# Optimization experiments

Hardware: AMD Instinct MI355X
Metric: run time of the kernel (lower is better)

Reference implementation:

```python
import jax, jax.numpy as jnp
import numpy as np

B, L, D, H = 4, 1024, 768, 12
DH = D // H  # 64


def setup_inputs() -> dict:
    key = jax.random.key(0)
    kx, kk, kq, kv = jax.random.split(key, 4)
    # Original uses torch.rand (uniform [0,1)); scale by 1/D so pre-softmax
    # logits stay in a numerically sane range (same math, better conditioning).
    scale = 1.0 / D
    x = jax.random.normal(kx, (B, L, D), dtype=jnp.float32)
    k = jax.random.uniform(kk, (H, D, D), dtype=jnp.float32) * scale
    q = jax.random.uniform(kq, (H, D, D), dtype=jnp.float32) * scale
    v = jax.random.uniform(kv, (H, DH, D), dtype=jnp.float32) * scale
    return {"x": x, "k": k, "q": q, "v": v}


def reference(x, k, q, v):
    # x: [B, L, D]; torch permutes to [B, D, L] then 'bdl,ncd->bncl';
    # equivalent directly: 'bld,ncd->bncl'.
    K = jnp.einsum('bld,ncd->bncl', x, k)   # [B, H, D, L]
    Q = jnp.einsum('bld,ncd->bncl', x, q)   # [B, H, D, L]
    V = jnp.einsum('bld,ncd->bncl', x, v)   # [B, H, DH, L]
    scores = jnp.einsum('bndl,bndm->bnlm', Q, K)        # [B, H, L, L]
    S = jax.nn.softmax(scores, axis=-1)                  # softmax over dim 3
    R = jnp.einsum('bnkl,bndl->bndk', S, V)              # [B, H, DH, L]
    R = R.reshape(x.shape[0], D, -1)                     # [B, D, L]
    return jnp.transpose(R, (0, 2, 1))                   # [B, L, D]
```

## Files before the change

kernel.cpp:

```cpp
#include <hip/hip_runtime.h>
#include <hip/hip_bf16.h>
#include <stdint.h>
#include <stddef.h>

typedef unsigned short u16;
typedef __attribute__((ext_vector_type(8))) short short8;
typedef __attribute__((ext_vector_type(4))) float f32x4;
typedef __attribute__((ext_vector_type(16))) float f32x16;

#define NB 4
#define NL 1024
#define ND 768
#define NH 12
#define NDH 64

__device__ __forceinline__ u16 f2bf(float f) {
  __hip_bfloat16 h = __float2bfloat16(f);
  return *reinterpret_cast<u16*>(&h);
}
__device__ __forceinline__ float bf2f(u16 u) {
  __hip_bfloat16 h;
  *reinterpret_cast<u16*>(&h) = u;
  return __bfloat162float(h);
}

__device__ __forceinline__ void load16_to_lds(const u16* g, u16* l) {
  __builtin_amdgcn_global_load_lds(
      (__attribute__((address_space(1))) void*)(uintptr_t)g,
      (__attribute__((address_space(3))) void*)(uint32_t)(uintptr_t)l,
      16, 0, 0);
}

__global__ __launch_bounds__(256) void cast2_bf16_kernel(const float* __restrict__ inA,
                                                         u16* __restrict__ outA, int n4A,
                                                         const float* __restrict__ inB,
                                                         u16* __restrict__ outB, int n4B) {
  int i = blockIdx.x * 256 + threadIdx.x;
  int stride = gridDim.x * 256;
  int tot = n4A + n4B;
  for (; i < tot; i += stride) {
    const float4* src;
    ushort4* dst;
    int j;
    if (i < n4A) { src = (const float4*)inA; dst = (ushort4*)outA; j = i; }
    else         { src = (const float4*)inB; dst = (ushort4*)outB; j = i - n4A; }
    float4 f = src[j];
    ushort4 o;
    o.x = f2bf(f.x); o.y = f2bf(f.y); o.z = f2bf(f.z); o.w = f2bf(f.w);
    dst[j] = o;
  }
}

__global__ __launch_bounds__(256) void transpose_cast2_kernel(const float* __restrict__ qI,
                                                              const float* __restrict__ kI,
                                                              u16* __restrict__ qT,
                                                              u16* __restrict__ kTp) {
  __shared__ float tile[32][33];
  int hz = blockIdx.z;
  int h = (hz < NH) ? hz : hz - NH;
  const float* src = ((hz < NH) ? qI : kI) + (size_t)h * ND * ND;
  u16* dst = ((hz < NH) ? qT : kTp) + (size_t)h * ND * ND;
  int c0 = blockIdx.x * 32, r0 = blockIdx.y * 32;
  int tx = threadIdx.x & 31, ty = threadIdx.x >> 5;
#pragma unroll
  for (int i = 0; i < 32; i += 8)
    tile[ty + i][tx] = src[(size_t)(r0 + ty + i) * ND + c0 + tx];
  __syncthreads();
  int p = tx & 15, j = (tx >> 4) * 8 + ty;
#pragma unroll
  for (int i = 0; i < 32; i += 16) {
    ushort2 o;
    o.x = f2bf(tile[2 * p][j + i]);
    o.y = f2bf(tile[2 * p + 1][j + i]);
    *(ushort2*)&dst[(size_t)(c0 + j + i) * ND + r0 + 2 * p] = o;
  }
}

template <bool BF16_OUT, int IM, int IN, int KDIM, int LDC>
__global__ __launch_bounds__(256, 4) void gemm_bt(
    const u16* __restrict__ A, const u16* __restrict__ Bm, void* __restrict__ Cv,
    long sAb, long sAn, long sAz,
    long sBb, long sBn, long sBz,
    long sCb, long sCn, long sCz,
    int p0) {
  constexpr int BK = 64;
  constexpr int MTILE = IM * 64;
  constexpr int NTILE = IN * 64;
  constexpr int CPR = BK / 8;
  constexpr int ACH = MTILE * CPR / 256;
  constexpr int BCH = NTILE * CPR / 256;
  __shared__ __align__(16) u16 As[MTILE * BK];
  __shared__ __align__(16) u16 Bs[NTILE * BK];

  int id = blockIdx.x + gridDim.x * (blockIdx.y + gridDim.y * blockIdx.z);
  int total = gridDim.x * gridDim.y * gridDim.z;
  int xx, yy, zz;
  if ((total & 7) == 0) {
    int per = total >> 3;
    int wk = (id & 7) * per + (id >> 3);
    xx = wk % gridDim.x;
    int g2 = wk / gridDim.x;
    yy = g2 % gridDim.y;
    zz = g2 / gridDim.y;
  } else {
    xx = blockIdx.x; yy = blockIdx.y; zz = blockIdx.z;
  }

  int g = p0 + zz;
  int b = g / NH, n = g % NH;
  A  += (size_t)b * sAb + (size_t)n * sAn + (size_t)zz * sAz;
  Bm += (size_t)b * sBb + (size_t)n * sBn + (size_t)zz * sBz;
  size_t cOff = (size_t)b * sCb + (size_t)n * sCn + (size_t)zz * sCz;

  int m0 = yy * MTILE, n0 = xx * NTILE;
  int t = threadIdx.x;
  int lane = t & 63, w = t >> 6;
  int m32 = lane & 31, kg = lane >> 5;
  int wm = w >> 1, wn = w & 1;

  const u16* gAb;
  const u16* gBb;
  {
    int r = t / CPR;
    int cc = (t & (CPR - 1)) ^ (r & 7);
    gAb = A + (size_t)(m0 + r) * KDIM + cc * 8;
    gBb = Bm + (size_t)(n0 + r) * KDIM + cc * 8;
  }

  f32x16 acc[IM][IN];
#pragma unroll
  for (int i = 0; i < IM; i++)
#pragma unroll
    for (int j = 0; j < IN; j++)
#pragma unroll
      for (int r = 0; r < 16; r++) acc[i][j][r] = 0.f;

#pragma unroll 1
  for (int k0 = 0; k0 < KDIM; k0 += BK) {
    __syncthreads();
#pragma unroll
    for (int u = 0; u < ACH; u++)
      load16_to_lds(gAb + (size_t)u * 32 * KDIM, &As[(size_t)(u * 256 + w * 64) * 8]);
    gAb += BK;
#pragma unroll
    for (int u = 0; u < BCH; u++)
      load16_to_lds(gBb + (size_t)u * 32 * KDIM, &Bs[(size_t)(u * 256 + w * 64) * 8]);
    gBb += BK;
    __syncthreads();

#pragma unroll
    for (int kc = 0; kc < 2; kc++) {
      short8 af[IM][2], bfr[IN][2];
#pragma unroll
      for (int i = 0; i < IM; i++) {
        int row = wm * (IM * 32) + i * 32 + m32;
#pragma unroll
        for (int h = 0; h < 2; h++) {
          int ck = (kc * 4 + h * 2 + kg) ^ (row & 7);
          af[i][h] = *(const short8*)&As[row * BK + ck * 8];
        }
      }
#pragma unroll
      for (int j = 0; j < IN; j++) {
        int row = wn * (IN * 32) + j * 32 + m32;
#pragma unroll
        for (int h = 0; h < 2; h++) {
          int ck = (kc * 4 + h * 2 + kg) ^ (row & 7);
          bfr[j][h] = *(const short8*)&Bs[row * BK + ck * 8];
        }
      }
#pragma unroll
      for (int i = 0; i < IM; i++)
#pragma unroll
        for (int j = 0; j < IN; j++) {
          acc[i][j] = __builtin_amdgcn_mfma_f32_32x32x16_bf16(af[i][0], bfr[j][0], acc[i][j], 0, 0, 0);
          acc[i][j] = __builtin_amdgcn_mfma_f32_32x32x16_bf16(af[i][1], bfr[j][1], acc[i][j], 0, 0, 0);
        }
    }
  }

#pragma unroll
  for (int i = 0; i < IM; i++) {
#pragma unroll
    for (int j = 0; j < IN; j++) {
      int colg = n0 + wn * (IN * 32) + j * 32 + m32;
#pragma unroll
      for (int r = 0; r < 16; r++) {
        int rowg = m0 + wm * (IM * 32) + i * 32 + (r & 3) + 8 * (r >> 2) + 4 * kg;
        float vv = acc[i][j][r];
        if (BF16_OUT) {
          ((u16*)Cv)[cOff + (size_t)rowg * LDC + colg] = f2bf(vv);
        } else {
          ((float*)Cv)[cOff + (size_t)rowg * LDC + colg] = vv;
        }
      }
    }
  }
}

__global__ __launch_bounds__(256, 4) void gemm_prep(
    const u16* __restrict__ kT, const u16* __restrict__ qT, u16* __restrict__ MTp,
    const u16* __restrict__ vb, const u16* __restrict__ xb, u16* __restrict__ V2p) {
  constexpr int BK = 64;
  constexpr int KDIM = ND;
  constexpr int CPR = BK / 8;
  constexpr long DD = (long)ND * ND;
  constexpr long LD = (long)NL * ND;
  __shared__ __align__(16) u16 As[128 * BK];
  __shared__ __align__(16) u16 Bs[128 * BK];

  int id = blockIdx.x + gridDim.x * (blockIdx.y + gridDim.y * blockIdx.z);
  int total = gridDim.x * gridDim.y * gridDim.z;
  int per = total >> 3;
  int wk = (id & 7) * per + (id >> 3);
  int xx = wk % gridDim.x;
  int g2 = wk / gridDim.x;
  int yy = g2 % gridDim.y;
  int zz = g2 / gridDim.y;

  const u16* A;
  const u16* Bm;
  u16* C;
  int ldc;
  if (zz < NH) {
    if (xx >= 6) return;
    A = kT + (size_t)zz * DD;
    Bm = qT + (size_t)zz * DD;
    C = MTp + (size_t)zz * DD;
    ldc = ND;
  } else {
    int b = zz - NH;
    A = vb;
    Bm = xb + (size_t)b * LD;
    C = V2p + (size_t)b * NH * NDH * NL;
    ldc = NL;
  }

  int m0 = yy * 128, n0 = xx * 128;
  int t = threadIdx.x;
  int lane = t & 63, w = t >> 6;
  int m32 = lane & 31, kg = lane >> 5;
  int wm = w >> 1, wn = w & 1;

  const u16* gAb;
  const u16* gBb;
  {
    int r = t / CPR;
    int cc = (t & (CPR - 1)) ^ (r & 7);
    gAb = A + (size_t)(m0 + r) * KDIM + cc * 8;
    gBb = Bm + (size_t)(n0 + r) * KDIM + cc * 8;
  }

  f32x16 acc[2][2];
#pragma unroll
  for (int i = 0; i < 2; i++)
#pragma unroll
    for (int j = 0; j < 2; j++)
#pragma unroll
      for (int r = 0; r < 16; r++) acc[i][j][r] = 0.f;

#pragma unroll 1
  for (int k0 = 0; k0 < KDIM; k0 += BK) {
    __syncthreads();
#pragma unroll
    for (int u = 0; u < 4; u++)
      load16_to_lds(gAb + (size_t)u * 32 * KDIM, &As[(size_t)(u * 256 + w * 64) * 8]);
    gAb += BK;
#pragma unroll
    for (int u = 0; u < 4; u++)
      load16_to_lds(gBb + (size_t)u * 32 * KDIM, &Bs[(size_t)(u * 256 + w * 64) * 8]);
    gBb += BK;
    __syncthreads();

#pragma unroll
    for (int kc = 0; kc < 2; kc++) {
      short8 af[2][2], bfr[2][2];
#pragma unroll
      for (int i = 0; i < 2; i++) {
        int row = wm * 64 + i * 32 + m32;
#pragma unroll
        for (int h = 0; h < 2; h++) {
          int ck = (kc * 4 + h * 2 + kg) ^ (row & 7);
          af[i][h] = *(const short8*)&As[row * BK + ck * 8];
        }
      }
#pragma unroll
      for (int j = 0; j < 2; j++) {
        int row = wn * 64 + j * 32 + m32;
#pragma unroll
        for (int h = 0; h < 2; h++) {
          int ck = (kc * 4 + h * 2 + kg) ^ (row & 7);
          bfr[j][h] = *(const short8*)&Bs[row * BK + ck * 8];
        }
      }
#pragma unroll
      for (int i = 0; i < 2; i++)
#pragma unroll
        for (int j = 0; j < 2; j++) {
          acc[i][j] = __builtin_amdgcn_mfma_f32_32x32x16_bf16(af[i][0], bfr[j][0], acc[i][j], 0, 0, 0);
          acc[i][j] = __builtin_amdgcn_mfma_f32_32x32x16_bf16(af[i][1], bfr[j][1], acc[i][j], 0, 0, 0);
        }
    }
  }

#pragma unroll
  for (int i = 0; i < 2; i++) {
#pragma unroll
    for (int j = 0; j < 2; j++) {
      int colg = n0 + wn * 64 + j * 32 + m32;
#pragma unroll
      for (int r = 0; r < 16; r++) {
        int rowg = m0 + wm * 64 + i * 32 + (r & 3) + 8 * (r >> 2) + 4 * kg;
        C[(size_t)rowg * ldc + colg] = f2bf(acc[i][j][r]);
      }
    }
  }
}

template <bool BF16_OUT, int KDIM, int LDC>
__global__ __launch_bounds__(512, 2) void gemm256_8p(
    const u16* __restrict__ A, const u16* __restrict__ Bm, void* __restrict__ Cv,
    long sAb, long sAn, long sAz,
    long sBb, long sBn, long sBz,
    long sCb, long sCn, long sCz,
    int p0) {
  constexpr int BK = 64;
  constexpr int NT = KDIM / BK;
  constexpr int NC = NT / 2;
  static_assert(KDIM % 128 == 0 && NC >= 2, "need even #K-tiles and >=2 cycles");
  __shared__ __align__(16) u16 As[2][256 * BK];
  __shared__ __align__(16) u16 Bs[2][256 * BK];

  int id = blockIdx.x + gridDim.x * (blockIdx.y + gridDim.y * blockIdx.z);
  int total = gridDim.x * gridDim.y * gridDim.z;
  int xx, yy, zz;
  if ((total & 7) == 0) {
    int per = total >> 3;
    int wk = (id & 7) * per + (id >> 3);
    xx = wk % gridDim.x;
    int g2 = wk / gridDim.x;
    yy = g2 % gridDim.y;
    zz = g2 / gridDim.y;
  } else {
    xx = blockIdx.x; yy = blockIdx.y; zz = blockIdx.z;
  }

  int g = p0 + zz;
  int b = g / NH, n = g % NH;
  A  += (size_t)b * sAb + (size_t)n * sAn + (size_t)zz * sAz;
  Bm += (size_t)b * sBb + (size_t)n * sBn + (size_t)zz * sBz;
  size_t cOff = (size_t)b * sCb + (size_t)n * sCn + (size_t)zz * sCz;

  int m0 = yy * 256, n0 = xx * 256;
  int t = threadIdx.x;
  int lane = t & 63, w = t >> 6;
  int wm = w >> 2, wn = w & 3;
  int l15 = lane & 15, q4 = lane >> 4;

  int r0 = t >> 3;
  int cc0 = (t & 7) ^ (r0 & 7);
  const u16* gA = A + (size_t)(m0 + r0) * KDIM + cc0 * 8;
  const u16* gB = Bm + (size_t)(n0 + r0) * KDIM + cc0 * 8;
  int wslab = w * 512;

#define STG_A1(d, h, u, kt) load16_to_lds( \
    gA + (size_t)((h) * 128 + (u) * 64) * KDIM + (size_t)(kt) * BK, \
    &As[d][((h) * 128 + (u) * 64) * BK + wslab])
#define STG_B1(d, h, u, kt) load16_to_lds( \
    gB + (size_t)((h) * 128 + (u) * 64) * KDIM + (size_t)(kt) * BK, \
    &Bs[d][((h) * 128 + (u) * 64) * BK + wslab])
#define STG_A2(d, h, kt) do { STG_A1(d, h, 0, kt); STG_A1(d, h, 1, kt); } while (0)
#define STG_B2(d, h, kt) do { STG_B1(d, h, 0, kt); STG_B1(d, h, 1, kt); } while (0)

#define READ_A(d, qm, dst) do { \
  _Pragma("unroll") for (int fm = 0; fm < 4; fm++) { \
    int row = (qm) * 128 + wm * 64 + fm * 16 + l15; \
    _Pragma("unroll") for (int ks = 0; ks < 2; ks++) { \
      int ck = (ks * 4 + q4) ^ (row & 7); \
      dst[fm][ks] = *(const short8*)&As[d][row * BK + ck * 8]; \
    } \
  } \
} while (0)

#define READ_B(d, qn, dst) do { \
  _Pragma("unroll") for (int fn = 0; fn < 2; fn++) { \
    int row = (qn) * 128 + wn * 32 + fn * 16 + l15; \
    _Pragma("unroll") for (int ks = 0; ks < 2; ks++) { \
      int ck = (ks * 4 + q4) ^ (row & 7); \
      dst[fn][ks] = *(const short8*)&Bs[d][row * BK + ck * 8]; \
    } \
  } \
} while (0)

#define MF_Q(qm, qn, AR, BR) do { \
  __builtin_amdgcn_s_setprio(1); \
  _Pragma("unroll") for (int ks = 0; ks < 2; ks++) \
    _Pragma("unroll") for (int fm = 0; fm < 4; fm++) \
      _Pragma("unroll") for (int fn = 0; fn < 2; fn++) \
        acc[qm][qn][fm][fn] = __builtin_amdgcn_mfma_f32_16x16x32_bf16( \
            AR[fm][ks], BR[fn][ks], acc[qm][qn][fm][fn], 0, 0, 0); \
  __builtin_amdgcn_s_setprio(0); \
} while (0)

#define PH_SYNC() do { \
  __builtin_amdgcn_s_barrier(); \
  asm volatile("s_waitcnt lgkmcnt(0)" ::: "memory"); \
  __builtin_amdgcn_sched_barrier(0); \
} while (0)
#define PH_END() do { \
  __builtin_amdgcn_s_barrier(); \
  __builtin_amdgcn_sched_barrier(0); \
} while (0)

  f32x4 acc[2][2][4][2];
#pragma unroll
  for (int qm = 0; qm < 2; qm++)
#pragma unroll
    for (int qn = 0; qn < 2; qn++)
#pragma unroll
      for (int fm = 0; fm < 4; fm++)
#pragma unroll
        for (int fn = 0; fn < 2; fn++)
          acc[qm][qn][fm][fn] = (f32x4){0.f, 0.f, 0.f, 0.f};

  STG_A2(0, 0, 0); STG_A2(0, 1, 0);
  STG_B2(0, 0, 0); STG_B2(0, 1, 0);
  STG_A2(1, 0, 1); STG_B2(1, 0, 1);
  asm volatile("s_waitcnt vmcnt(4)" ::: "memory");
  __builtin_amdgcn_s_barrier();
  __builtin_amdgcn_sched_barrier(0);

#pragma unroll 1
  for (int cyc = 0; cyc < NC; ++cyc) {
    int t0 = cyc * 2;
    bool full = (cyc + 1 < NC);
    short8 af0[4][2], af1[4][2], bq0[2][2], bq1[2][2];

    READ_A(0, 0, af0); READ_B(0, 0, bq0);
    STG_A2(1, 1, t0 + 1);
    PH_SYNC(); MF_Q(0, 0, af0, bq0); PH_END();
    READ_B(0, 1, bq1);
    STG_B2(1, 1, t0 + 1);
    PH_SYNC(); MF_Q(0, 1, af0, bq1); PH_END();
    READ_A(0, 1, af1);
    if (full) STG_A2(0, 0, t0 + 2);
    PH_SYNC(); MF_Q(1, 0, af1, bq0); PH_END();
    if (full) STG_B2(0, 0, t0 + 2);
    __builtin_amdgcn_s_barrier();
    MF_Q(1, 1, af1, bq1);
    __builtin_amdgcn_sched_barrier(0);
    if (full) asm volatile("s_waitcnt vmcnt(4)" ::: "memory");
    else      asm volatile("s_waitcnt vmcnt(0)" ::: "memory");
    PH_END();

    READ_A(1, 0, af0); READ_B(1, 0, bq0);
    if (full) STG_A2(0, 1, t0 + 2);
    PH_SYNC(); MF_Q(0, 0, af0, bq0); PH_END();
    READ_B(1, 1, bq1);
    if (full) STG_B2(0, 1, t0 + 2);
    PH_SYNC(); MF_Q(0, 1, af0, bq1); PH_END();
    READ_A(1, 1, af1);
    if (full) STG_A2(1, 0, t0 + 3);
    PH_SYNC(); MF_Q(1, 0, af1, bq0); PH_END();
    if (full) {
      STG_B2(1, 0, t0 + 3);
      __builtin_amdgcn_s_barrier();
      MF_Q(1, 1, af1, bq1);
      __builtin_amdgcn_sched_barrier(0);
      asm volatile("s_waitcnt vmcnt(4)" ::: "memory");
      PH_END();
    } else {
      __builtin_amdgcn_s_barrier();
      MF_Q(1, 1, af1, bq1);
    }
  }

#pragma unroll
  for (int qm = 0; qm < 2; qm++)
#pragma unroll
    for (int qn = 0; qn < 2; qn++)
#pragma unroll
      for (int fm = 0; fm < 4; fm++)
#pragma unroll
        for (int fn = 0; fn < 2; fn++) {
          int colg = n0 + qn * 128 + wn * 32 + fn * 16 + l15;
#pragma unroll
          for (int r = 0; r < 4; r++) {
            int rowg = m0 + qm * 128 + wm * 64 + fm * 16 + q4 * 4 + r;
            float vv = acc[qm][qn][fm][fn][r];
            if (BF16_OUT) {
              ((u16*)Cv)[cOff + (size_t)rowg * LDC + colg] = f2bf(vv);
            } else {
              ((float*)Cv)[cOff + (size_t)rowg * LDC + colg] = vv;
            }
          }
        }
#undef STG_A1
#undef STG_B1
#undef STG_A2
#undef STG_B2
#undef READ_A
#undef READ_B
#undef MF_Q
#undef PH_SYNC
#undef PH_END
}

__global__ __launch_bounds__(256) void softmax_pv_kernel(
    const u16* __restrict__ Sb, const u16* __restrict__ V2, float* __restrict__ out,
    int p0) {
  __shared__ __align__(16) u16 Ps[64 * 128];
  __shared__ __align__(16) u16 Vs[64 * 128];

  int id = blockIdx.x + gridDim.x * blockIdx.y;
  int total = gridDim.x * gridDim.y;
  int xx, zz;
  if ((total & 7) == 0) {
    int per = total >> 3;
    int wk = (id & 7) * per + (id >> 3);
    xx = wk & 15; zz = wk >> 4;
  } else {
    xx = blockIdx.x; zz = blockIdx.y;
  }

  int g = p0 + zz;
  int b = g / NH, n = g % NH;
  const u16* S = Sb + (size_t)zz * NL * NL;
  const u16* V = V2 + (size_t)g * NDH * NL;

  int l0 = xx * 64;
  int t = threadIdx.x;
  int lane = t & 63, w = t >> 6;
  int row16 = lane & 15, q = lane >> 4;
  int rs = row16 & 7;

  f32x4 acc[5];
#pragma unroll
  for (int j = 0; j < 5; j++) acc[j] = (f32x4){0.f, 0.f, 0.f, 0.f};

  short8 onesf;
  {
    short val = (row16 == 0) ? (short)0x3F80 : (short)0;
#pragma unroll
    for (int e = 0; e < 8; e++) onesf[e] = val;
  }

  const u16* ssrc[4];
  const u16* vsrc[4];
#pragma unroll
  for (int u = 0; u < 4; u++) {
    int c = u * 256 + t;
    int r = c >> 4, cc = (c & 15) ^ (r & 7);
    ssrc[u] = S + (size_t)(l0 + r) * NL + cc * 8;
    vsrc[u] = V + (size_t)r * NL + cc * 8;
  }

#pragma unroll 1
  for (int mt = 0; mt < 8; mt++) {
    int mo = mt * 128;
    __syncthreads();
#pragma unroll
    for (int u = 0; u < 4; u++)
      load16_to_lds(ssrc[u] + mo, &Ps[(size_t)(u * 256 + w * 64) * 8]);
#pragma unroll
    for (int u = 0; u < 4; u++)
      load16_to_lds(vsrc[u] + mo, &Vs[(size_t)(u * 256 + w * 64) * 8]);
    __syncthreads();

#pragma unroll
    for (int kk = 0; kk < 4; kk++) {
      int ch = ((kk * 4 + q) ^ rs) * 16;
      int lrow = w * 16 + row16;
      short8 raw = *(const short8*)((const char*)Ps + lrow * 256 + ch);
      short8 af;
#pragma unroll
      for (int e = 0; e < 8; e++) af[e] = (short)f2bf(__expf(bf2f((u16)raw[e])));
      short8 bfr[4];
#pragma unroll
      for (int j = 0; j < 4; j++) {
        int dh = j * 16 + row16;
        bfr[j] = *(const short8*)((const char*)Vs + dh * 256 + ch);
      }
#pragma unroll
      for (int j = 0; j < 4; j++)
        acc[j] = __builtin_amdgcn_mfma_f32_16x16x32_bf16(af, bfr[j], acc[j], 0, 0, 0);
      acc[4] = __builtin_amdgcn_mfma_f32_16x16x32_bf16(af, onesf, acc[4], 0, 0, 0);
    }
  }

#pragma unroll
  for (int r = 0; r < 4; r++) {
    float sum = __shfl(acc[4][r], lane & 48, 64);
    float inv = 1.0f / sum;
    int row = l0 + w * 16 + q * 4 + r;
    float* op = out + ((size_t)b * NL + row) * ND + n * NDH;
#pragma unroll
    for (int j = 0; j < 4; j++)
      op[j * 16 + row16] = acc[j][r] * inv;
  }
}

extern "C" void kernel_launch(void* const* d_in, const int* in_sizes, int n_in,
                              void* d_out, int out_size, void* d_ws, size_t ws_size,
                              hipStream_t stream) {
  (void)in_sizes; (void)n_in; (void)out_size;
  const float* x  = (const float*)d_in[0];
  const float* kI = (const float*)d_in[1];
  const float* qI = (const float*)d_in[2];
  const float* vI = (const float*)d_in[3];
  float* out = (float*)d_out;

  size_t off = 0;
  char* wsb = (char*)d_ws;
  auto alloc = [&](size_t bytes) -> char* {
    char* p = wsb + off;
    off += (bytes + 255) & ~(size_t)255;
    return p;
  };
  u16* xb = (u16*)alloc((size_t)NB * NL * ND * 2);
  u16* vb = (u16*)alloc((size_t)NH * NDH * ND * 2);
  u16* MT = (u16*)alloc((size_t)NH * ND * ND * 2);
  u16* V2 = (u16*)alloc((size_t)NB * NH * NDH * NL * 2);
  size_t fixedSz = off;

  u16* qT = (u16*)alloc((size_t)NH * ND * ND * 2);
  u16* kT = (u16*)alloc((size_t)NH * ND * ND * 2);
  size_t scratchEndQK = off;

  const size_t Tsz  = (size_t)NL * ND * 2;
  const size_t Ssz  = (size_t)NL * NL * 2;
  const size_t perPair = Tsz + Ssz;

  int chunk = NB * NH;
  {
    size_t avail = ws_size > fixedSz ? ws_size - fixedSz : 0;
    size_t maxChunk = avail / perPair;
    if (maxChunk < 1) maxChunk = 1;
    if (maxChunk < (size_t)chunk) {
      int passes = (int)(((size_t)NB * NH + maxChunk - 1) / maxChunk);
      chunk = (NB * NH + passes - 1) / passes;
    }
  }
  off = fixedSz;
  u16* T  = (u16*)alloc((size_t)chunk * Tsz);
  u16* Sb = (u16*)alloc((size_t)chunk * Ssz);
  if (off < scratchEndQK) off = scratchEndQK;

  const long DD  = (long)ND * ND;
  const long LD  = (long)NL * ND;
  const long LL  = (long)NL * NL;

  {
    int n4A = NB * NL * ND / 4;
    int n4B = NH * NDH * ND / 4;
    cast2_bf16_kernel<<<dim3((n4A + n4B + 255) / 256), dim3(256), 0, stream>>>(
        x, xb, n4A, vI, vb, n4B);
  }
  transpose_cast2_kernel<<<dim3(24, 24, 2 * NH), dim3(256), 0, stream>>>(qI, kI, qT, kT);

  gemm_prep<<<dim3(8, 6, 16), dim3(256), 0, stream>>>(kT, qT, MT, vb, xb, V2);

  for (int p0 = 0; p0 < NB * NH; p0 += chunk) {
    int c = NB * NH - p0;
    if (c > chunk) c = chunk;
    gemm_bt<true, 2, 2, 768, ND><<<dim3(6, 8, c), dim3(256), 0, stream>>>(
        xb, MT, T,
        LD, 0, 0,  0, DD, 0,  0, 0, LD, p0);
    gemm256_8p<true, 768, NL><<<dim3(4, 4, c), dim3(512), 0, stream>>>(
        T, xb, Sb,
        0, 0, LD,  LD, 0, 0,  0, 0, LL, p0);
    softmax_pv_kernel<<<dim3(16, c), dim3(256), 0, stream>>>(Sb, V2, out, p0);
  }
}
```

Baseline: 300.7 us.

## Fuse QK score GEMM into softmax-PV kernel, dropping the score matrix buffer

```diff
diff --git a/kernel.cpp b/kernel.cpp
--- a/kernel.cpp
+++ b/kernel.cpp
@@ -317,198 +317,12 @@
   }
 }
 
-template <bool BF16_OUT, int KDIM, int LDC>
-__global__ __launch_bounds__(512, 2) void gemm256_8p(
-    const u16* __restrict__ A, const u16* __restrict__ Bm, void* __restrict__ Cv,
-    long sAb, long sAn, long sAz,
-    long sBb, long sBn, long sBz,
-    long sCb, long sCn, long sCz,
-    int p0) {
+__global__ __launch_bounds__(256, 2) void qk_softmax_pv(
+    const u16* __restrict__ Tq, const u16* __restrict__ xb, const u16* __restrict__ V2,
+    float* __restrict__ out, int p0) {
   constexpr int BK = 64;
-  constexpr int NT = KDIM / BK;
-  constexpr int NC = NT / 2;
-  static_assert(KDIM % 128 == 0 && NC >= 2, "need even #K-tiles and >=2 cycles");
-  __shared__ __align__(16) u16 As[2][256 * BK];
-  __shared__ __align__(16) u16 Bs[2][256 * BK];
-
-  int id = blockIdx.x + gridDim.x * (blockIdx.y + gridDim.y * blockIdx.z);
-  int total = gridDim.x * gridDim.y * gridDim.z;
-  int xx, yy, zz;
-  if ((total & 7) == 0) {
-    int per = total >> 3;
-    int wk = (id & 7) * per + (id >> 3);
-    xx = wk % gridDim.x;
-    int g2 = wk / gridDim.x;
-    yy = g2 % gridDim.y;
-    zz = g2 / gridDim.y;
-  } else {
-    xx = blockIdx.x; yy = blockIdx.y; zz = blockIdx.z;
-  }
-
-  int g = p0 + zz;
-  int b = g / NH, n = g % NH;
-  A  += (size_t)b * sAb + (size_t)n * sAn + (size_t)zz * sAz;
-  Bm += (size_t)b * sBb + (size_t)n * sBn + (size_t)zz * sBz;
-  size_t cOff = (size_t)b * sCb + (size_t)n * sCn + (size_t)zz * sCz;
-
-  int m0 = yy * 256, n0 = xx * 256;
-  int t = threadIdx.x;
-  int lane = t & 63, w = t >> 6;
-  int wm = w >> 2, wn = w & 3;
-  int l15 = lane & 15, q4 = lane >> 4;
-
-  int r0 = t >> 3;
-  int cc0 = (t & 7) ^ (r0 & 7);
-  const u16* gA = A + (size_t)(m0 + r0) * KDIM + cc0 * 8;
-  const u16* gB = Bm + (size_t)(n0 + r0) * KDIM + cc0 * 8;
-  int wslab = w * 512;
-
-#define STG_A1(d, h, u, kt) load16_to_lds( \
-    gA + (size_t)((h) * 128 + (u) * 64) * KDIM + (size_t)(kt) * BK, \
-    &As[d][((h) * 128 + (u) * 64) * BK + wslab])
-#define STG_B1(d, h, u, kt) load16_to_lds( \
-    gB + (size_t)((h) * 128 + (u) * 64) * KDIM + (size_t)(kt) * BK, \
-    &Bs[d][((h) * 128 + (u) * 64) * BK + wslab])
-#define STG_A2(d, h, kt) do { STG_A1(d, h, 0, kt); STG_A1(d, h, 1, kt); } while (0)
-#define STG_B2(d, h, kt) do { STG_B1(d, h, 0, kt); STG_B1(d, h, 1, kt); } while (0)
-
-#define READ_A(d, qm, dst) do { \
-  _Pragma("unroll") for (int fm = 0; fm < 4; fm++) { \
-    int row = (qm) * 128 + wm * 64 + fm * 16 + l15; \
-    _Pragma("unroll") for (int ks = 0; ks < 2; ks++) { \
-      int ck = (ks * 4 + q4) ^ (row & 7); \
-      dst[fm][ks] = *(const short8*)&As[d][row * BK + ck * 8]; \
-    } \
-  } \
-} while (0)
-
-#define READ_B(d, qn, dst) do { \
-  _Pragma("unroll") for (int fn = 0; fn < 2; fn++) { \
-    int row = (qn) * 128 + wn * 32 + fn * 16 + l15; \
-    _Pragma("unroll") for (int ks = 0; ks < 2; ks++) { \
-      int ck = (ks * 4 + q4) ^ (row & 7); \
-      dst[fn][ks] = *(const short8*)&Bs[d][row * BK + ck * 8]; \
-    } \
-  } \
-} while (0)
-
-#define MF_Q(qm, qn, AR, BR) do { \
-  __builtin_amdgcn_s_setprio(1); \
-  _Pragma("unroll") for (int ks = 0; ks < 2; ks++) \
-    _Pragma("unroll") for (int fm = 0; fm < 4; fm++) \
-      _Pragma("unroll") for (int fn = 0; fn < 2; fn++) \
-        acc[qm][qn][fm][fn] = __builtin_amdgcn_mfma_f32_16x16x32_bf16( \
-            AR[fm][ks], BR[fn][ks], acc[qm][qn][fm][fn], 0, 0, 0); \
-  __builtin_amdgcn_s_setprio(0); \
-} while (0)
-
-#define PH_SYNC() do { \
-  __builtin_amdgcn_s_barrier(); \
-  asm volatile("s_waitcnt lgkmcnt(0)" ::: "memory"); \
-  __builtin_amdgcn_sched_barrier(0); \
-} while (0)
-#define PH_END() do { \
-  __builtin_amdgcn_s_barrier(); \
-  __builtin_amdgcn_sched_barrier(0); \
-} while (0)
-
-  f32x4 acc[2][2][4][2];
-#pragma unroll
-  for (int qm = 0; qm < 2; qm++)
-#pragma unroll
-    for (int qn = 0; qn < 2; qn++)
-#pragma unroll
-      for (int fm = 0; fm < 4; fm++)
-#pragma unroll
-        for (int fn = 0; fn < 2; fn++)
-          acc[qm][qn][fm][fn] = (f32x4){0.f, 0.f, 0.f, 0.f};
-
-  STG_A2(0, 0, 0); STG_A2(0, 1, 0);
-  STG_B2(0, 0, 0); STG_B2(0, 1, 0);
-  STG_A2(1, 0, 1); STG_B2(1, 0, 1);
-  asm volatile("s_waitcnt vmcnt(4)" ::: "memory");
-  __builtin_amdgcn_s_barrier();
-  __builtin_amdgcn_sched_barrier(0);
-
-#pragma unroll 1
-  for (int cyc = 0; cyc < NC; ++cyc) {
-    int t0 = cyc * 2;
-    bool full = (cyc + 1 < NC);
-    short8 af0[4][2], af1[4][2], bq0[2][2], bq1[2][2];
-
-    READ_A(0, 0, af0); READ_B(0, 0, bq0);
-    STG_A2(1, 1, t0 + 1);
-    PH_SYNC(); MF_Q(0, 0, af0, bq0); PH_END();
-    READ_B(0, 1, bq1);
-    STG_B2(1, 1, t0 + 1);
-    PH_SYNC(); MF_Q(0, 1, af0, bq1); PH_END();
-    READ_A(0, 1, af1);
-    if (full) STG_A2(0, 0, t0 + 2);
-    PH_SYNC(); MF_Q(1, 0, af1, bq0); PH_END();
-    if (full) STG_B2(0, 0, t0 + 2);
-    __builtin_amdgcn_s_barrier();
-    MF_Q(1, 1, af1, bq1);
-    __builtin_amdgcn_sched_barrier(0);
-    if (full) asm volatile("s_waitcnt vmcnt(4)" ::: "memory");
-    else      asm volatile("s_waitcnt vmcnt(0)" ::: "memory");
-    PH_END();
-
-    READ_A(1, 0, af0); READ_B(1, 0, bq0);
-    if (full) STG_A2(0, 1, t0 + 2);
-    PH_SYNC(); MF_Q(0, 0, af0, bq0); PH_END();
-    READ_B(1, 1, bq1);
-    if (full) STG_B2(0, 1, t0 + 2);
-    PH_SYNC(); MF_Q(0, 1, af0, bq1); PH_END();
-    READ_A(1, 1, af1);
-    if (full) STG_A2(1, 0, t0 + 3);
-    PH_SYNC(); MF_Q(1, 0, af1, bq0); PH_END();
-    if (full) {
-      STG_B2(1, 0, t0 + 3);
-      __builtin_amdgcn_s_barrier();
-      MF_Q(1, 1, af1, bq1);
-      __builtin_amdgcn_sched_barrier(0);
-      asm volatile("s_waitcnt vmcnt(4)" ::: "memory");
-      PH_END();
-    } else {
-      __builtin_amdgcn_s_barrier();
-      MF_Q(1, 1, af1, bq1);
-    }
-  }
-
-#pragma unroll
-  for (int qm = 0; qm < 2; qm++)
-#pragma unroll
-    for (int qn = 0; qn < 2; qn++)
-#pragma unroll
-      for (int fm = 0; fm < 4; fm++)
-#pragma unroll
-        for (int fn = 0; fn < 2; fn++) {
-          int colg = n0 + qn * 128 + wn * 32 + fn * 16 + l15;
-#pragma unroll
-          for (int r = 0; r < 4; r++) {
-            int rowg = m0 + qm * 128 + wm * 64 + fm * 16 + q4 * 4 + r;
-            float vv = acc[qm][qn][fm][fn][r];
-            if (BF16_OUT) {
-              ((u16*)Cv)[cOff + (size_t)rowg * LDC + colg] = f2bf(vv);
-            } else {
-              ((float*)Cv)[cOff + (size_t)rowg * LDC + colg] = vv;
-            }
-          }
-        }
-#undef STG_A1
-#undef STG_B1
-#undef STG_A2
-#undef STG_B2
-#undef READ_A
-#undef READ_B
-#undef MF_Q
-#undef PH_SYNC
-#undef PH_END
-}
-
-__global__ __launch_bounds__(256) void softmax_pv_kernel(
-    const u16* __restrict__ Sb, const u16* __restrict__ V2, float* __restrict__ out,
-    int p0) {
+  __shared__ __align__(16) u16 As[64 * BK];
+  __shared__ __align__(16) u16 Bs[128 * BK];
   __shared__ __align__(16) u16 Ps[64 * 128];
   __shared__ __align__(16) u16 Vs[64 * 128];
 
@@ -525,14 +339,28 @@
 
   int g = p0 + zz;
   int b = g / NH, n = g % NH;
-  const u16* S = Sb + (size_t)zz * NL * NL;
-  const u16* V = V2 + (size_t)g * NDH * NL;
-
-  int l0 = xx * 64;
+  const u16* Tz = Tq + (size_t)zz * NL * ND + (size_t)(xx * 64) * ND;
+  const u16* Xb = xb + (size_t)b * NL * ND;
+  const u16* V  = V2 + (size_t)g * NDH * NL;
+
   int t = threadIdx.x;
   int lane = t & 63, w = t >> 6;
-  int row16 = lane & 15, q = lane >> 4;
+  int m32 = lane & 31, kg = lane >> 5;
+  int wm = w >> 1, wn = w & 1;
+  int row16 = lane & 15, q4 = lane >> 4;
   int rs = row16 & 7;
+
+  int r8 = t >> 3;
+  int cc8 = (t & 7) ^ (r8 & 7);
+  const u16* gA = Tz + (size_t)r8 * ND + cc8 * 8;
+  const u16* gB = Xb + (size_t)r8 * ND + cc8 * 8;
+  const u16* vsrc[4];
+#pragma unroll
+  for (int u = 0; u < 4; u++) {
+    int c = u * 256 + t;
+    int r = c >> 4, cc = (c & 15) ^ (r & 7);
+    vsrc[u] = V + (size_t)r * NL + cc * 8;
+  }
 
   f32x4 acc[5];
 #pragma unroll
@@ -545,46 +373,83 @@
     for (int e = 0; e < 8; e++) onesf[e] = val;
   }
 
-  const u16* ssrc[4];
-  const u16* vsrc[4];
-#pragma unroll
-  for (int u = 0; u < 4; u++) {
-    int c = u * 256 + t;
-    int r = c >> 4, cc = (c & 15) ^ (r & 7);
-    ssrc[u] = S + (size_t)(l0 + r) * NL + cc * 8;
-    vsrc[u] = V + (size_t)r * NL + cc * 8;
-  }
-
 #pragma unroll 1
   for (int mt = 0; mt < 8; mt++) {
-    int mo = mt * 128;
+    const u16* gBm = gB + (size_t)mt * 128 * ND;
+    f32x16 qacc[2];
+#pragma unroll
+    for (int j = 0; j < 2; j++)
+#pragma unroll
+      for (int r = 0; r < 16; r++) qacc[j][r] = 0.f;
+
+#pragma unroll 1
+    for (int k0 = 0; k0 < ND; k0 += BK) {
+      __syncthreads();
+#pragma unroll
+      for (int u = 0; u < 2; u++)
+        load16_to_lds(gA + (size_t)u * 32 * ND + k0, &As[(size_t)(u * 256 + w * 64) * 8]);
+#pragma unroll
+      for (int u = 0; u < 4; u++)
+        load16_to_lds(gBm + (size_t)u * 32 * ND + k0, &Bs[(size_t)(u * 256 + w * 64) * 8]);
+      __syncthreads();
+
+#pragma unroll
+      for (int kc = 0; kc < 2; kc++) {
+        short8 af[2], bfr[2][2];
+        int rowa = wm * 32 + m32;
+#pragma unroll
+        for (int h = 0; h < 2; h++) {
+          int ck = (kc * 4 + h * 2 + kg) ^ (rowa & 7);
+          af[h] = *(const short8*)&As[rowa * BK + ck * 8];
+        }
+#pragma unroll
+        for (int j = 0; j < 2; j++) {
+          int rowb = wn * 64 + j * 32 + m32;
+#pragma unroll
+          for (int h = 0; h < 2; h++) {
+            int ck = (kc * 4 + h * 2 + kg) ^ (rowb & 7);
+            bfr[j][h] = *(const short8*)&Bs[rowb * BK + ck * 8];
+          }
+        }
+#pragma unroll
+        for (int j = 0; j < 2; j++) {
+          qacc[j] = __builtin_amdgcn_mfma_f32_32x32x16_bf16(af[0], bfr[j][0], qacc[j], 0, 0, 0);
+          qacc[j] = __builtin_amdgcn_mfma_f32_32x32x16_bf16(af[1], bfr[j][1], qacc[j], 0, 0, 0);
+        }
+      }
+    }
+
+#pragma unroll
+    for (int u = 0; u < 4; u++)
+      load16_to_lds(vsrc[u] + mt * 128, &Vs[(size_t)(u * 256 + w * 64) * 8]);
+
+#pragma unroll
+    for (int j = 0; j < 2; j++) {
+      int m = wn * 64 + j * 32 + m32;
+#pragma unroll
+      for (int r = 0; r < 16; r++) {
+        int l = wm * 32 + (r & 3) + 8 * (r >> 2) + 4 * kg;
+        int byteoff = l * 256 + (((m >> 3) ^ (l & 7)) * 16) + (m & 7) * 2;
+        *(u16*)((char*)Ps + byteoff) = f2bf(__expf(qacc[j][r]));
+      }
+    }
     __syncthreads();
-#pragma unroll
-    for (int u = 0; u < 4; u++)
-      load16_to_lds(ssrc[u] + mo, &Ps[(size_t)(u * 256 + w * 64) * 8]);
-#pragma unroll
-    for (int u = 0; u < 4; u++)
-      load16_to_lds(vsrc[u] + mo, &Vs[(size_t)(u * 256 + w * 64) * 8]);
-    __syncthreads();
 
 #pragma unroll
     for (int kk = 0; kk < 4; kk++) {
-      int ch = ((kk * 4 + q) ^ rs) * 16;
+      int ch = ((kk * 4 + q4) ^ rs) * 16;
       int lrow = w * 16 + row16;
-      short8 raw = *(const short8*)((const char*)Ps + lrow * 256 + ch);
-      short8 af;
-#pragma unroll
-      for (int e = 0; e < 8; e++) af[e] = (short)f2bf(__expf(bf2f((u16)raw[e])));
-      short8 bfr[4];
+      short8 paf = *(const short8*)((const char*)Ps + lrow * 256 + ch);
+      short8 bfr2[4];
 #pragma unroll
       for (int j = 0; j < 4; j++) {
         int dh = j * 16 + row16;
-        bfr[j] = *(const short8*)((const char*)Vs + dh * 256 + ch);
+        bfr2[j] = *(const short8*)((const char*)Vs + dh * 256 + ch);
       }
 #pragma unroll
       for (int j = 0; j < 4; j++)
-        acc[j] = __builtin_amdgcn_mfma_f32_16x16x32_bf16(af, bfr[j], acc[j], 0, 0, 0);
-      acc[4] = __builtin_amdgcn_mfma_f32_16x16x32_bf16(af, onesf, acc[4], 0, 0, 0);
+        acc[j] = __builtin_amdgcn_mfma_f32_16x16x32_bf16(paf, bfr2[j], acc[j], 0, 0, 0);
+      acc[4] = __builtin_amdgcn_mfma_f32_16x16x32_bf16(paf, onesf, acc[4], 0, 0, 0);
     }
   }
 
@@ -592,7 +457,7 @@
   for (int r = 0; r < 4; r++) {
     float sum = __shfl(acc[4][r], lane & 48, 64);
     float inv = 1.0f / sum;
-    int row = l0 + w * 16 + q * 4 + r;
+    int row = xx * 64 + w * 16 + q4 * 4 + r;
     float* op = out + ((size_t)b * NL + row) * ND + n * NDH;
 #pragma unroll
     for (int j = 0; j < 4; j++)
@@ -627,14 +492,12 @@
   u16* kT = (u16*)alloc((size_t)NH * ND * ND * 2);
   size_t scratchEndQK = off;
 
-  const size_t Tsz  = (size_t)NL * ND * 2;
-  const size_t Ssz  = (size_t)NL * NL * 2;
-  const size_t perPair = Tsz + Ssz;
+  const size_t Tsz = (size_t)NL * ND * 2;
 
   int chunk = NB * NH;
   {
     size_t avail = ws_size > fixedSz ? ws_size - fixedSz : 0;
-    size_t maxChunk = avail / perPair;
+    size_t maxChunk = avail / Tsz;
     if (maxChunk < 1) maxChunk = 1;
     if (maxChunk < (size_t)chunk) {
       int passes = (int)(((size_t)NB * NH + maxChunk - 1) / maxChunk);
@@ -642,13 +505,11 @@
     }
   }
   off = fixedSz;
-  u16* T  = (u16*)alloc((size_t)chunk * Tsz);
-  u16* Sb = (u16*)alloc((size_t)chunk * Ssz);
+  u16* T = (u16*)alloc((size_t)chunk * Tsz);
   if (off < scratchEndQK) off = scratchEndQK;
 
-  const long DD  = (long)ND * ND;
-  const long LD  = (long)NL * ND;
-  const long LL  = (long)NL * NL;
+  const long DD = (long)ND * ND;
+  const long LD = (long)NL * ND;
 
   {
     int n4A = NB * NL * ND / 4;
@@ -666,9 +527,6 @@
     gemm_bt<true, 2, 2, 768, ND><<<dim3(6, 8, c), dim3(256), 0, stream>>>(
         xb, MT, T,
         LD, 0, 0,  0, DD, 0,  0, 0, LD, p0);
-    gemm256_8p<true, 768, NL><<<dim3(4, 4, c), dim3(512), 0, stream>>>(
-        T, xb, Sb,
-        0, 0, LD,  LD, 0, 0,  0, 0, LL, p0);
-    softmax_pv_kernel<<<dim3(16, c), dim3(256), 0, stream>>>(Sb, V2, out, p0);
-  }
-}
+    qk_softmax_pv<<<dim3(16, c), dim3(256), 0, stream>>>(T, xb, V2, out, p0);
+  }
+}
```

After: 363.9 us. +21.0%, slower.

## Fuse exp into score GEMM epilogue and merge input prep kernels

Applied to the files above, without the earlier changes.

```diff
diff --git a/kernel.cpp b/kernel.cpp
--- a/kernel.cpp
+++ b/kernel.cpp
@@ -31,32 +31,30 @@
       16, 0, 0);
 }
 
-__global__ __launch_bounds__(256) void cast2_bf16_kernel(const float* __restrict__ inA,
-                                                         u16* __restrict__ outA, int n4A,
-                                                         const float* __restrict__ inB,
-                                                         u16* __restrict__ outB, int n4B) {
-  int i = blockIdx.x * 256 + threadIdx.x;
-  int stride = gridDim.x * 256;
-  int tot = n4A + n4B;
-  for (; i < tot; i += stride) {
-    const float4* src;
-    ushort4* dst;
-    int j;
-    if (i < n4A) { src = (const float4*)inA; dst = (ushort4*)outA; j = i; }
-    else         { src = (const float4*)inB; dst = (ushort4*)outB; j = i - n4A; }
-    float4 f = src[j];
-    ushort4 o;
-    o.x = f2bf(f.x); o.y = f2bf(f.y); o.z = f2bf(f.z); o.w = f2bf(f.w);
-    dst[j] = o;
-  }
-}
-
-__global__ __launch_bounds__(256) void transpose_cast2_kernel(const float* __restrict__ qI,
-                                                              const float* __restrict__ kI,
-                                                              u16* __restrict__ qT,
-                                                              u16* __restrict__ kTp) {
+__global__ __launch_bounds__(256) void prep_inputs_kernel(
+    const float* __restrict__ qI, const float* __restrict__ kI,
+    u16* __restrict__ qT, u16* __restrict__ kTp,
+    const float* __restrict__ x, u16* __restrict__ xb, int n4A,
+    const float* __restrict__ vI, u16* __restrict__ vb, int n4B) {
   __shared__ float tile[32][33];
   int hz = blockIdx.z;
+  if (hz == 2 * NH) {
+    int i = (blockIdx.x + 24 * blockIdx.y) * 256 + threadIdx.x;
+    int stride = 576 * 256;
+    int tot = n4A + n4B;
+    for (; i < tot; i += stride) {
+      const float4* src;
+      ushort4* dst;
+      int j;
+      if (i < n4A) { src = (const float4*)x; dst = (ushort4*)xb; j = i; }
+      else         { src = (const float4*)vI; dst = (ushort4*)vb; j = i - n4A; }
+      float4 f = src[j];
+      ushort4 o;
+      o.x = f2bf(f.x); o.y = f2bf(f.y); o.z = f2bf(f.z); o.w = f2bf(f.w);
+      dst[j] = o;
+    }
+    return;
+  }
   int h = (hz < NH) ? hz : hz - NH;
   const float* src = ((hz < NH) ? qI : kI) + (size_t)h * ND * ND;
   u16* dst = ((hz < NH) ? qT : kTp) + (size_t)h * ND * ND;
@@ -317,7 +315,7 @@
   }
 }
 
-template <bool BF16_OUT, int KDIM, int LDC>
+template <int OUTMODE, int KDIM, int LDC>
 __global__ __launch_bounds__(512, 2) void gemm256_8p(
     const u16* __restrict__ A, const u16* __restrict__ Bm, void* __restrict__ Cv,
     long sAb, long sAn, long sAz,
@@ -488,7 +486,8 @@
           for (int r = 0; r < 4; r++) {
             int rowg = m0 + qm * 128 + wm * 64 + fm * 16 + q4 * 4 + r;
             float vv = acc[qm][qn][fm][fn][r];
-            if (BF16_OUT) {
+            if (OUTMODE == 2) vv = __expf(vv);
+            if (OUTMODE >= 1) {
               ((u16*)Cv)[cOff + (size_t)rowg * LDC + colg] = f2bf(vv);
             } else {
               ((float*)Cv)[cOff + (size_t)rowg * LDC + colg] = vv;
@@ -507,7 +506,7 @@
 }
 
 __global__ __launch_bounds__(256) void softmax_pv_kernel(
-    const u16* __restrict__ Sb, const u16* __restrict__ V2, float* __restrict__ out,
+    const u16* __restrict__ Pb, const u16* __restrict__ V2, float* __restrict__ out,
     int p0) {
   __shared__ __align__(16) u16 Ps[64 * 128];
   __shared__ __align__(16) u16 Vs[64 * 128];
@@ -525,7 +524,7 @@
 
   int g = p0 + zz;
   int b = g / NH, n = g % NH;
-  const u16* S = Sb + (size_t)zz * NL * NL;
+  const u16* S = Pb + (size_t)zz * NL * NL;
   const u16* V = V2 + (size_t)g * NDH * NL;
 
   int l0 = xx * 64;
@@ -571,10 +570,7 @@
     for (int kk = 0; kk < 4; kk++) {
       int ch = ((kk * 4 + q) ^ rs) * 16;
       int lrow = w * 16 + row16;
-      short8 raw = *(const short8*)((const char*)Ps + lrow * 256 + ch);
-      short8 af;
-#pragma unroll
-      for (int e = 0; e < 8; e++) af[e] = (short)f2bf(__expf(bf2f((u16)raw[e])));
+      short8 paf = *(const short8*)((const char*)Ps + lrow * 256 + ch);
       short8 bfr[4];
 #pragma unroll
       for (int j = 0; j < 4; j++) {
@@ -583,8 +579,8 @@
       }
 #pragma unroll
       for (int j = 0; j < 4; j++)
-        acc[j] = __builtin_amdgcn_mfma_f32_16x16x32_bf16(af, bfr[j], acc[j], 0, 0, 0);
-      acc[4] = __builtin_amdgcn_mfma_f32_16x16x32_bf16(af, onesf, acc[4], 0, 0, 0);
+        acc[j] = __builtin_amdgcn_mfma_f32_16x16x32_bf16(paf, bfr[j], acc[j], 0, 0, 0);
+      acc[4] = __builtin_amdgcn_mfma_f32_16x16x32_bf16(paf, onesf, acc[4], 0, 0, 0);
     }
   }
 
@@ -653,10 +649,9 @@
   {
     int n4A = NB * NL * ND / 4;
     int n4B = NH * NDH * ND / 4;
-    cast2_bf16_kernel<<<dim3((n4A + n4B + 255) / 256), dim3(256), 0, stream>>>(
-        x, xb, n4A, vI, vb, n4B);
-  }
-  transpose_cast2_kernel<<<dim3(24, 24, 2 * NH), dim3(256), 0, stream>>>(qI, kI, qT, kT);
+    prep_inputs_kernel<<<dim3(24, 24, 2 * NH + 1), dim3(256), 0, stream>>>(
+        qI, kI, qT, kT, x, xb, n4A, vI, vb, n4B);
+  }
 
   gemm_prep<<<dim3(8, 6, 16), dim3(256), 0, stream>>>(kT, qT, MT, vb, xb, V2);
 
@@ -666,7 +661,7 @@
     gemm_bt<true, 2, 2, 768, ND><<<dim3(6, 8, c), dim3(256), 0, stream>>>(
         xb, MT, T,
         LD, 0, 0,  0, DD, 0,  0, 0, LD, p0);
-    gemm256_8p<true, 768, NL><<<dim3(4, 4, c), dim3(512), 0, stream>>>(
+    gemm256_8p<2, 768, NL><<<dim3(4, 4, c), dim3(512), 0, stream>>>(
         T, xb, Sb,
         0, 0, LD,  LD, 0, 0,  0, 0, LL, p0);
     softmax_pv_kernel<<<dim3(16, c), dim3(256), 0, stream>>>(Sb, V2, out, p0);
```

Result: faster. 290.8 us (median of 2 runs) (-3.3%).
